# Performance work log

Hardware: AMD Instinct MI355X
Metric: run time of the kernel (lower is better)

Reference implementation:

```python
import jax, jax.numpy as jnp
import numpy as np
from jax import lax

B, CIN, H, W = 32, 1, 128, 128
SC, CC = 128, 128          # simple / complex channels
C = SC + CC                # 256
KS, STRIDE, PAD = 5, 2, 2  # gabor conv
KDN = 1                    # dn kernel half-size -> 3x3
K_EXC = 25.0
DN = ('NCHW', 'OIHW', 'NCHW')


def _make_gaussian_bank(key):
    k1, k2, k3, k4 = jax.random.split(key, 4)
    thetaD = jnp.abs(jax.random.normal(k1, (C, C)))
    p = jnp.abs(jax.random.normal(k2, (C, C)))
    sig = jnp.abs(jax.random.normal(k3, (C, C)))
    a = jnp.abs(jax.random.normal(k4, (C, C)))
    lin = jnp.linspace(-KDN, KDN, 2 * KDN + 1)
    xv, yv = jnp.meshgrid(lin, lin, indexing='ij')  # torch.meshgrid default 'ij'
    ct = jnp.cos(thetaD)[..., None, None]
    st = jnp.sin(thetaD)[..., None, None]
    xrot = xv * ct + yv * st                        # (C, C, 3, 3)
    yrot = -xv * st + yv * ct
    amp = (a / (2.0 * jnp.pi * p * sig))[..., None, None]
    p2 = (p ** 2)[..., None, None]
    s2 = (sig ** 2)[..., None, None]
    return amp * jnp.exp(-0.5 * (xrot ** 2 / p2 + yrot ** 2 / s2))


def setup_inputs() -> dict:
    key = jax.random.key(0)
    kx, k0, k1, kg = jax.random.split(key, 4)
    x = jax.random.normal(kx, (B, CIN, H, W), dtype=jnp.float32)
    w_q0 = 0.1 * jax.random.normal(k0, (C, CIN, KS, KS), dtype=jnp.float32)
    w_q1 = 0.1 * jax.random.normal(k1, (C, CIN, KS, KS), dtype=jnp.float32)
    gaussian_bank = _make_gaussian_bank(kg).astype(jnp.float32)
    return {"x": x, "w_q0": w_q0, "w_q1": w_q1, "gaussian_bank": gaussian_bank}


def reference(x, w_q0, w_q1, gaussian_bank):
    # Gabor filter bank: two quadrature convs, stride 2, pad 2
    q0 = lax.conv_general_dilated(x, w_q0, (STRIDE, STRIDE),
                                  [(PAD, PAD), (PAD, PAD)], dimension_numbers=DN)
    q1 = lax.conv_general_dilated(x, w_q1, (STRIDE, STRIDE),
                                  [(PAD, PAD), (PAD, PAD)], dimension_numbers=DN)
    s = jax.nn.relu(q0[:, :SC])                                  # simple cells
    c = jnp.sqrt(q0[:, SC:] ** 2 + q1[:, SC:] ** 2) / jnp.sqrt(2.0).astype(x.dtype)
    y = K_EXC * jnp.concatenate((s, c), axis=1)                  # (B, C, 64, 64)
    y = jax.nn.relu(y)                                           # noise_mode=None -> just relu
    # Divisive normalization: gaussian-weighted cross-channel pooling, then divide
    under = lax.conv_general_dilated(y, gaussian_bank, (1, 1),
                                     [(KDN, KDN), (KDN, KDN)], dimension_numbers=DN)
    return y / under
```

## Files before the change

### kernel.cpp

```cpp
#include <hip/hip_runtime.h>
#include <cstddef>


#define NSC 128
#define GSCALE 64.0f

typedef short s8v __attribute__((ext_vector_type(8)));
typedef float f4v __attribute__((ext_vector_type(4)));
typedef _Float16 h8v __attribute__((ext_vector_type(8)));

__device__ __forceinline__ short f2h(float f) {
    return __builtin_bit_cast(short, (_Float16)f);
}
__device__ __forceinline__ float h2f(short s) {
    return (float)__builtin_bit_cast(_Float16, s);
}

__global__ __launch_bounds__(256) void prep_g(const float* __restrict__ g,
                                              short* __restrict__ gf) {
    int t = blockIdx.x * 256 + threadIdx.x;
    int co = t & 255, ci = (t >> 8) & 255, kxy = t >> 16;
    float v = g[((size_t)co * 256 + ci) * 9 + kxy] * (1.0f / GSCALE);
    v = fminf(v, 65504.f);
    int wv = co >> 6, m = (co >> 4) & 3, i = co & 15;
    int cc = ci >> 5, q = (ci >> 3) & 3, j = ci & 7;
    int l = q * 16 + i;
    size_t base = ((((size_t)(kxy * 4 + wv) * 4 + m) * 8 + cc)) * 512 + (size_t)l * 8 + j;
    gf[base] = f2h(v);
}

__global__ __launch_bounds__(256) void gabor(const float* __restrict__ x,
                                             const float* __restrict__ wq0,
                                             const float* __restrict__ wq1,
                                             short* __restrict__ y2) {
    __shared__ float xbuf[5][132];
    int oh = blockIdx.x, b = blockIdx.y, c = threadIdx.x;
    for (int i = c; i < 5 * 132; i += 256) (&xbuf[0][0])[i] = 0.f;
    __syncthreads();
    int ihb = oh * 2 - 2;
    for (int i = c; i < 5 * 128; i += 256) {
        int r = i >> 7, col = i & 127;
        int ih = ihb + r;
        if ((unsigned)ih < 128u)
            xbuf[r][col + 2] = x[((size_t)b * 128 + ih) * 128 + col];
    }
    short* yb = y2 + ((size_t)(b * 64 + oh) * 64) * 512 + c;

    if (c < NSC) {
        float w0[25];
#pragma unroll
        for (int i = 0; i < 25; ++i) w0[i] = wq0[c * 25 + i];
        __syncthreads();
        for (int og = 0; og < 16; ++og) {
            int cb = og * 8;
            float q0[4] = {0.f, 0.f, 0.f, 0.f};
#pragma unroll
            for (int ky = 0; ky < 5; ++ky) {
                float xr[12];
                *(float4*)&xr[0] = *(const float4*)&xbuf[ky][cb];
                *(float4*)&xr[4] = *(const float4*)&xbuf[ky][cb + 4];
                *(float4*)&xr[8] = *(const float4*)&xbuf[ky][cb + 8];
#pragma unroll
                for (int j = 0; j < 4; ++j)
#pragma unroll
                    for (int kx = 0; kx < 5; ++kx)
                        q0[j] = fmaf(w0[ky * 5 + kx], xr[2 * j + kx], q0[j]);
            }
#pragma unroll
            for (int j = 0; j < 4; ++j) {
                float v = 25.f * fmaxf(q0[j], 0.f);
                short hi = f2h(v);
                short lo = f2h(v - h2f(hi));
                int ow = og * 4 + j;
                yb[(size_t)ow * 512] = hi;
                yb[(size_t)ow * 512 + 256] = lo;
            }
        }
    } else {
        float w0[25], w1[25];
#pragma unroll
        for (int i = 0; i < 25; ++i) w0[i] = wq0[c * 25 + i];
#pragma unroll
        for (int i = 0; i < 25; ++i) w1[i] = wq1[c * 25 + i];
        __syncthreads();
        for (int og = 0; og < 16; ++og) {
            int cb = og * 8;
            float q0[4] = {0.f, 0.f, 0.f, 0.f}, q1[4] = {0.f, 0.f, 0.f, 0.f};
#pragma unroll
            for (int ky = 0; ky < 5; ++ky) {
                float xr[12];
                *(float4*)&xr[0] = *(const float4*)&xbuf[ky][cb];
                *(float4*)&xr[4] = *(const float4*)&xbuf[ky][cb + 4];
                *(float4*)&xr[8] = *(const float4*)&xbuf[ky][cb + 8];
#pragma unroll
                for (int j = 0; j < 4; ++j)
#pragma unroll
                    for (int kx = 0; kx < 5; ++kx) {
                        q0[j] = fmaf(w0[ky * 5 + kx], xr[2 * j + kx], q0[j]);
                        q1[j] = fmaf(w1[ky * 5 + kx], xr[2 * j + kx], q1[j]);
                    }
            }
#pragma unroll
            for (int j = 0; j < 4; ++j) {
                float v = 25.f * sqrtf(fmaf(q0[j], q0[j], q1[j] * q1[j])) * 0.70710678118654752f;
                short hi = f2h(v);
                short lo = f2h(v - h2f(hi));
                int ow = og * 4 + j;
                yb[(size_t)ow * 512] = hi;
                yb[(size_t)ow * 512 + 256] = lo;
            }
        }
    }
}

__device__ __forceinline__ void stage_row(const short* __restrict__ y2,
                                          short* __restrict__ bh,
                                          int b, int r, int half, int tid) {
    if ((unsigned)r < 64u) {
        const float4* rowbase = (const float4*)(y2 + (size_t)((b * 64 + r) * 64) * 512);
#pragma unroll
        for (int p4 = 0; p4 < 4; ++p4) {
            int i = p4 * 256 + tid;
            int w = i >> 4, gr = i & 15;
            float4 vh = rowbase[(size_t)w * 64 + half * 16 + gr];
            *(float4*)&bh[(w + 1) * 136 + gr * 8] = vh;
        }
    } else {
#pragma unroll
        for (int p4 = 0; p4 < 4; ++p4) {
            int i = p4 * 256 + tid;
            int w = i >> 4, gr = i & 15;
            *(float4*)&bh[(w + 1) * 136 + gr * 8] = (float4){0.f, 0.f, 0.f, 0.f};
        }
    }
}

__global__ __launch_bounds__(256, 2) void dn(const short* __restrict__ y2,
                                             const short* __restrict__ gf,
                                             float* __restrict__ out) {
    __shared__ short bhi[2][66 * 136];
    int h = blockIdx.x * 2, b = blockIdx.y;
    int tid = threadIdx.x;
    int wv = tid >> 6, l = tid & 63;
    int li = l & 15, lq = l >> 4;

    if (tid < 64) {
        int buf = (tid >> 5) & 1;
        int row = (tid >> 4) & 1, gr = tid & 15;
        *(float4*)&bhi[buf][(row ? 65 : 0) * 136 + gr * 8] = (float4){0.f, 0.f, 0.f, 0.f};
    }

    f4v acc[2][4][4];
#pragma unroll
    for (int hs = 0; hs < 2; ++hs)
#pragma unroll
        for (int m = 0; m < 4; ++m)
#pragma unroll
            for (int n = 0; n < 4; ++n)
                acc[hs][m][n] = (f4v){0.f, 0.f, 0.f, 0.f};

    const h8v* GA = (const h8v*)gf;

    for (int half = 0; half < 2; ++half) {
        for (int ky = 0; ky < 3; ++ky) {
            int r0 = h + ky - 1, r1 = h + ky;
            __syncthreads();
            if (ky == 0)
                stage_row(y2, bhi[r0 & 1], b, r0, half, tid);
            stage_row(y2, bhi[r1 & 1], b, r1, half, tid);
            __syncthreads();
            const h8v* BH0 = (const h8v*)bhi[r0 & 1];
            const h8v* BH1 = (const h8v*)bhi[r1 & 1];

            for (int kx = 0; kx < 3; ++kx) {
                int kxy = ky * 3 + kx;
#pragma unroll
                for (int cc = 0; cc < 4; ++cc) {
                    int ccg = half * 4 + cc;
                    h8v Ah[4];
#pragma unroll
                    for (int m = 0; m < 4; ++m) {
                        size_t ab = ((((size_t)(kxy * 4 + wv) * 4 + m) * 8 + ccg)) * 64 + l;
                        Ah[m] = GA[ab];
                    }
#pragma unroll
                    for (int hs = 0; hs < 2; ++hs) {
                        const h8v* BH = hs ? BH1 : BH0;
                        h8v Bh[4];
#pragma unroll
                        for (int nt = 0; nt < 4; ++nt) {
                            int gidx = (nt * 16 + li + kx) * 17 + cc * 4 + lq;
                            Bh[nt] = BH[gidx];
                        }
#pragma unroll
                        for (int m = 0; m < 4; ++m)
#pragma unroll
                            for (int nt = 0; nt < 4; ++nt)
                                acc[hs][m][nt] = __builtin_amdgcn_mfma_f32_16x16x32_f16(Ah[m], Bh[nt], acc[hs][m][nt], 0, 0, 0);
                    }
                }
            }
        }
    }

#pragma unroll
    for (int hs = 0; hs < 2; ++hs) {
        const short* nrow = y2 + (size_t)((b * 64 + h + hs) * 64) * 512;
#pragma unroll
        for (int m = 0; m < 4; ++m) {
            int co = wv * 64 + m * 16 + lq * 4;
#pragma unroll
            for (int nt = 0; nt < 4; ++nt) {
                int w = nt * 16 + li;
                const short* np = nrow + (size_t)w * 512 + co;
                ushort4 nh = *(const ushort4*)np;
                ushort4 nl = *(const ushort4*)(np + 256);
                float n0 = h2f((short)nh.x) + h2f((short)nl.x);
                float n1 = h2f((short)nh.y) + h2f((short)nl.y);
                float n2 = h2f((short)nh.z) + h2f((short)nl.z);
                float n3 = h2f((short)nh.w) + h2f((short)nl.w);
                size_t ob = ((size_t)(b * 256 + co) * 64 + (h + hs)) * 64 + w;
                out[ob]            = n0 / (GSCALE * acc[hs][m][nt][0]);
                out[ob + 4096]     = n1 / (GSCALE * acc[hs][m][nt][1]);
                out[ob + 2 * 4096] = n2 / (GSCALE * acc[hs][m][nt][2]);
                out[ob + 3 * 4096] = n3 / (GSCALE * acc[hs][m][nt][3]);
            }
        }
    }
}

extern "C" void kernel_launch(void* const* d_in, const int* in_sizes, int n_in,
                              void* d_out, int out_size, void* d_ws, size_t ws_size,
                              hipStream_t stream) {
    const float* x   = (const float*)d_in[0];
    const float* wq0 = (const float*)d_in[1];
    const float* wq1 = (const float*)d_in[2];
    const float* g   = (const float*)d_in[3];
    float* out = (float*)d_out;
    short* y2 = (short*)d_ws;
    short* gf = y2 + 67108864;

    prep_g<<<2304, 256, 0, stream>>>(g, gf);
    gabor<<<dim3(64, 32), 256, 0, stream>>>(x, wq0, wq1, y2);
    dn<<<dim3(32, 32), 256, 0, stream>>>(y2, gf, out);
}
```

Baseline: 336.8 us.

## Triple-buffer DN row staging with register prefetch and XOR-swizzled LDS layout

Replaces the two-slot LDS row buffer with a three-slot ring. The global load for the next input row is issued into registers before the MFMA loop and written to LDS only after the loop, so global latency overlaps compute and each ky step needs one barrier instead of two. The padded 136-short row layout is replaced by an unpadded layout with an XOR swizzle on the 16-byte group index, applied at load time, to avoid LDS bank conflicts. This holds 16 extra registers of staging data per thread under a 2-blocks-per-SM launch bound and uses slightly more shared memory.

```diff
diff --git a/kernel.cpp b/kernel.cpp
--- a/kernel.cpp
+++ b/kernel.cpp
@@ -5,7 +5,6 @@
 #define NSC 128
 #define GSCALE 64.0f
 
-typedef short s8v __attribute__((ext_vector_type(8)));
 typedef float f4v __attribute__((ext_vector_type(4)));
 typedef _Float16 h8v __attribute__((ext_vector_type(8)));
 
@@ -113,41 +112,45 @@
     }
 }
 
-__device__ __forceinline__ void stage_row(const short* __restrict__ y2,
-                                          short* __restrict__ bh,
-                                          int b, int r, int half, int tid) {
+__device__ __forceinline__ void stage_load(const short* __restrict__ y2, float4* sr,
+                                           int b, int r, int half, int tid) {
     if ((unsigned)r < 64u) {
-        const float4* rowbase = (const float4*)(y2 + (size_t)((b * 64 + r) * 64) * 512);
+        const short* rowbase = y2 + (size_t)((b * 64 + r) * 64) * 512;
 #pragma unroll
         for (int p4 = 0; p4 < 4; ++p4) {
             int i = p4 * 256 + tid;
-            int w = i >> 4, gr = i & 15;
-            float4 vh = rowbase[(size_t)w * 64 + half * 16 + gr];
-            *(float4*)&bh[(w + 1) * 136 + gr * 8] = vh;
+            int w66 = (i >> 4) + 1, g = i & 15;
+            int sg = ((w66 - 1) << 6) + half * 16 + (g ^ (w66 & 7));
+            sr[p4] = *(const float4*)(rowbase + (size_t)sg * 8);
         }
     } else {
 #pragma unroll
-        for (int p4 = 0; p4 < 4; ++p4) {
-            int i = p4 * 256 + tid;
-            int w = i >> 4, gr = i & 15;
-            *(float4*)&bh[(w + 1) * 136 + gr * 8] = (float4){0.f, 0.f, 0.f, 0.f};
-        }
+        for (int p4 = 0; p4 < 4; ++p4) sr[p4] = (float4){0.f, 0.f, 0.f, 0.f};
+    }
+}
+
+__device__ __forceinline__ void stage_write(short* __restrict__ buf, const float4* sr,
+                                            int tid) {
+#pragma unroll
+    for (int p4 = 0; p4 < 4; ++p4) {
+        int i = p4 * 256 + tid;
+        *(float4*)(buf + (size_t)(16 + i) * 8) = sr[p4];
     }
 }
 
 __global__ __launch_bounds__(256, 2) void dn(const short* __restrict__ y2,
                                              const short* __restrict__ gf,
                                              float* __restrict__ out) {
-    __shared__ short bhi[2][66 * 136];
+    __shared__ short bbuf[3][66 * 16 * 8];
     int h = blockIdx.x * 2, b = blockIdx.y;
     int tid = threadIdx.x;
     int wv = tid >> 6, l = tid & 63;
     int li = l & 15, lq = l >> 4;
 
-    if (tid < 64) {
-        int buf = (tid >> 5) & 1;
-        int row = (tid >> 4) & 1, gr = tid & 15;
-        *(float4*)&bhi[buf][(row ? 65 : 0) * 136 + gr * 8] = (float4){0.f, 0.f, 0.f, 0.f};
+    if (tid < 96) {
+        int bi = tid >> 5, t2 = tid & 31;
+        int row = (t2 >> 4) ? 65 : 0, g = t2 & 15;
+        *(float4*)&bbuf[bi][(row * 16 + g) * 8] = (float4){0.f, 0.f, 0.f, 0.f};
     }
 
     f4v acc[2][4][4];
@@ -162,15 +165,19 @@
     const h8v* GA = (const h8v*)gf;
 
     for (int half = 0; half < 2; ++half) {
+        float4 sr[4];
+        stage_load(y2, sr, b, h - 1, half, tid);
+        stage_write(bbuf[(h + 2) % 3], sr, tid);
+        stage_load(y2, sr, b, h, half, tid);
+        stage_write(bbuf[h % 3], sr, tid);
+        __syncthreads();
+
         for (int ky = 0; ky < 3; ++ky) {
-            int r0 = h + ky - 1, r1 = h + ky;
-            __syncthreads();
-            if (ky == 0)
-                stage_row(y2, bhi[r0 & 1], b, r0, half, tid);
-            stage_row(y2, bhi[r1 & 1], b, r1, half, tid);
-            __syncthreads();
-            const h8v* BH0 = (const h8v*)bhi[r0 & 1];
-            const h8v* BH1 = (const h8v*)bhi[r1 & 1];
+            if (ky < 2)
+                stage_load(y2, sr, b, h + ky + 1, half, tid);
+
+            const h8v* B0 = (const h8v*)bbuf[(h + ky + 2) % 3];
+            const h8v* B1 = (const h8v*)bbuf[(h + ky) % 3];
 
             for (int kx = 0; kx < 3; ++kx) {
                 int kxy = ky * 3 + kx;
@@ -185,12 +192,13 @@
                     }
 #pragma unroll
                     for (int hs = 0; hs < 2; ++hs) {
-                        const h8v* BH = hs ? BH1 : BH0;
+                        const h8v* BH = hs ? B1 : B0;
                         h8v Bh[4];
 #pragma unroll
                         for (int nt = 0; nt < 4; ++nt) {
-                            int gidx = (nt * 16 + li + kx) * 17 + cc * 4 + lq;
-                            Bh[nt] = BH[gidx];
+                            int w66 = nt * 16 + li + kx;
+                            int g = (cc * 4 + lq) ^ (w66 & 7);
+                            Bh[nt] = BH[w66 * 16 + g];
                         }
 #pragma unroll
                         for (int m = 0; m < 4; ++m)
@@ -200,6 +208,10 @@
                     }
                 }
             }
+
+            if (ky < 2)
+                stage_write(bbuf[(h + ky + 1) % 3], sr, tid);
+            __syncthreads();
         }
     }
 
```

New measurement: 325.0 us. -3.5%, faster.
